# Kernel tuning notes

Hardware: AMD Instinct MI355X
Metric: run time of the kernel (lower is better)

## Reference

```python
import jax, jax.numpy as jnp
import numpy as np

N_POINTS = 1 << 20      # batch of query coordinates
IN_CH = 3               # 3D coordinates in [0,1]
N_FREQ = 8              # Fourier encoding frequencies
ENC_CH = IN_CH + 2 * IN_CH * N_FREQ   # identity + sin/cos -> 51
HIDDEN = 64
OUT_CH = 4


def _fourier_encode(x):
    # x: [N, 3] in [0,1]. Identity + NeRF-style frequency encoding.
    freqs = (2.0 ** jnp.arange(N_FREQ, dtype=x.dtype)) * jnp.pi      # [L]
    xf = x[:, :, None] * freqs                                       # [N, 3, L]
    n = x.shape[0]
    return jnp.concatenate(
        [x, jnp.sin(xf).reshape(n, -1), jnp.cos(xf).reshape(n, -1)], axis=-1
    )  # [N, 51]


def setup_inputs() -> dict:
    key = jax.random.key(0)
    ks = jax.random.split(key, 9)
    inp = jax.random.uniform(ks[0], (N_POINTS, IN_CH), dtype=jnp.float32)

    def _w(k, fan_out, fan_in):
        scale = jnp.sqrt(2.0 / fan_in).astype(jnp.float32)
        return jax.random.normal(k, (fan_out, fan_in), dtype=jnp.float32) * scale

    return {
        "input": inp,
        "W0": _w(ks[1], HIDDEN, ENC_CH), "b0": jnp.zeros((HIDDEN,), jnp.float32),
        "W1": _w(ks[2], HIDDEN, HIDDEN), "b1": jnp.zeros((HIDDEN,), jnp.float32),
        "W2": _w(ks[3], HIDDEN, HIDDEN), "b2": jnp.zeros((HIDDEN,), jnp.float32),
        "W3": _w(ks[4], OUT_CH, HIDDEN), "b3": jnp.zeros((OUT_CH,), jnp.float32),
    }


def reference(input, W0, b0, W1, b1, W2, b2, W3, b3):
    h = _fourier_encode(input)                       # [N, 51]
    h = jax.nn.relu(h @ W0.T + b0)                   # [N, 64]
    h = jax.nn.relu(h @ W1.T + b1)                   # [N, 64]
    h = jax.nn.relu(h @ W2.T + b2)                   # [N, 64]
    return h @ W3.T + b3                             # [N, 4]
```

## Files before the change

### kernel.cpp

```cpp
#include <hip/hip_runtime.h>
#include <cmath>


typedef _Float16 half8 __attribute__((ext_vector_type(8)));
typedef float float4v __attribute__((ext_vector_type(4)));

#define PI_F 3.14159265358979323846f

template <int KIN, int ROWS, bool RELU, bool LAST>
__device__ __forceinline__ void mlp_layer(const float* __restrict__ W,
                                          const float* __restrict__ bias,
                                          float* __restrict__ hb,
                                          float* __restrict__ outp,
                                          long long wbase, int lane, long long n)
{
    const int l15 = lane & 15;
    const int g   = lane >> 4;

    half8 Ah[4][2], Al[4][2];
#pragma unroll
    for (int m = 0; m < 4; ++m) {
        const int row = 16 * m + l15;
#pragma unroll
        for (int c = 0; c < 2; ++c) {
            const int v0 = (8 * c + 2 * g) ^ l15;
            const int v1 = (8 * c + 2 * g + 1) ^ l15;
            float4v r0 = *(const float4v*)&hb[row * 64 + v0 * 4];
            float4v r1 = *(const float4v*)&hb[row * 64 + v1 * 4];
#pragma unroll
            for (int j = 0; j < 4; ++j) {
                float v = r0[j];
                _Float16 hi = (_Float16)v;
                Ah[m][c][j] = hi;
                Al[m][c][j] = (_Float16)(v - (float)hi);
                float w = r1[j];
                _Float16 hw = (_Float16)w;
                Ah[m][c][4 + j] = hw;
                Al[m][c][4 + j] = (_Float16)(w - (float)hw);
            }
        }
    }

    constexpr int NT = (ROWS + 15) / 16;
#pragma unroll
    for (int nt = 0; nt < NT; ++nt) {
        const int j = 16 * nt + l15;
        const float bj = (j < ROWS) ? bias[j] : 0.f;

        half8 Bh[2], Bl[2];
#pragma unroll
        for (int c = 0; c < 2; ++c) {
            if constexpr (KIN == 64 && ROWS == 64) {
                const float4v* Wv = (const float4v*)(W + j * 64 + 32 * c + 8 * g);
                float4v w0 = Wv[0], w1 = Wv[1];
#pragma unroll
                for (int jj = 0; jj < 4; ++jj) {
                    float w = w0[jj];
                    _Float16 hi = (_Float16)w;
                    Bh[c][jj] = hi; Bl[c][jj] = (_Float16)(w - (float)hi);
                    float w2 = w1[jj];
                    _Float16 h2 = (_Float16)w2;
                    Bh[c][4 + jj] = h2; Bl[c][4 + jj] = (_Float16)(w2 - (float)h2);
                }
            } else {
#pragma unroll
                for (int jj = 0; jj < 8; ++jj) {
                    const int k = 32 * c + 8 * g + jj;
                    float w = (j < ROWS && k < KIN) ? W[j * KIN + k] : 0.f;
                    _Float16 hi = (_Float16)w;
                    Bh[c][jj] = hi; Bl[c][jj] = (_Float16)(w - (float)hi);
                }
            }
        }

#pragma unroll
        for (int m = 0; m < 4; ++m) {
            float4v acc = {bj, bj, bj, bj};
#pragma unroll
            for (int c = 0; c < 2; ++c) {
                acc = __builtin_amdgcn_mfma_f32_16x16x32_f16(Ah[m][c], Bh[c], acc, 0, 0, 0);
                acc = __builtin_amdgcn_mfma_f32_16x16x32_f16(Ah[m][c], Bl[c], acc, 0, 0, 0);
                acc = __builtin_amdgcn_mfma_f32_16x16x32_f16(Al[m][c], Bh[c], acc, 0, 0, 0);
            }
            if constexpr (LAST) {
                if (l15 < 4) {
#pragma unroll
                    for (int r = 0; r < 4; ++r) {
                        long long p = wbase + 16 * m + 4 * g + r;
                        if (p < n) outp[p * 4 + l15] = acc[r];
                    }
                }
            } else {
#pragma unroll
                for (int r = 0; r < 4; ++r) {
                    float v = acc[r];
                    if (RELU) v = fmaxf(v, 0.f);
                    const int row = 16 * m + 4 * g + r;
                    const int col = 16 * nt + l15;
                    hb[row * 64 + ((((col >> 2) ^ (row & 15))) << 2) + (col & 3)] = v;
                }
            }
        }
    }
}

__global__ __launch_bounds__(256)
void fused_mlp_mfma(const float* __restrict__ x,
                    const float* __restrict__ W0, const float* __restrict__ b0,
                    const float* __restrict__ W1, const float* __restrict__ b1,
                    const float* __restrict__ W2, const float* __restrict__ b2,
                    const float* __restrict__ W3, const float* __restrict__ b3,
                    float* __restrict__ out, long long n)
{
    __shared__ float hbuf[4][64 * 64];
    const int tid  = threadIdx.x;
    const int wave = tid >> 6;
    const int lane = tid & 63;
    const int l15  = lane & 15;
    float* hb = hbuf[wave];

    const long long wbase = (long long)blockIdx.x * 256 + wave * 64;

    {
        long long p = wbase + lane;
        if (p > n - 1) p = n - 1;
        float xc[3] = {x[3 * p + 0], x[3 * p + 1], x[3 * p + 2]};
        float e[64];
        e[0] = xc[0]; e[1] = xc[1]; e[2] = xc[2];
#pragma unroll
        for (int ch = 0; ch < 3; ++ch) {
#pragma unroll
            for (int f = 0; f < 8; ++f) {
                float s, c;
                sincosf(xc[ch] * (PI_F * (float)(1 << f)), &s, &c);
                e[3 + ch * 8 + f]  = s;
                e[27 + ch * 8 + f] = c;
            }
        }
#pragma unroll
        for (int k = 51; k < 64; ++k) e[k] = 0.f;
#pragma unroll
        for (int cb = 0; cb < 16; ++cb) {
            float4v v = {e[4 * cb], e[4 * cb + 1], e[4 * cb + 2], e[4 * cb + 3]};
            *(float4v*)&hb[lane * 64 + ((cb ^ l15) << 2)] = v;
        }
    }

    mlp_layer<51, 64, true,  false>(W0, b0, hb, nullptr, wbase, lane, n);
    mlp_layer<64, 64, true,  false>(W1, b1, hb, nullptr, wbase, lane, n);
    mlp_layer<64, 64, true,  false>(W2, b2, hb, nullptr, wbase, lane, n);
    mlp_layer<64, 4,  false, true >(W3, b3, hb, out,     wbase, lane, n);
}

extern "C" void kernel_launch(void* const* d_in, const int* in_sizes, int n_in,
                              void* d_out, int out_size, void* d_ws, size_t ws_size,
                              hipStream_t stream)
{
    const float* x  = (const float*)d_in[0];
    const float* W0 = (const float*)d_in[1];
    const float* b0 = (const float*)d_in[2];
    const float* W1 = (const float*)d_in[3];
    const float* b1 = (const float*)d_in[4];
    const float* W2 = (const float*)d_in[5];
    const float* b2 = (const float*)d_in[6];
    const float* W3 = (const float*)d_in[7];
    const float* b3 = (const float*)d_in[8];
    float* out = (float*)d_out;

    const long long n = in_sizes[0] / 3;
    const int block = 256;
    const int grid = (int)((n + 255) / 256);
    fused_mlp_mfma<<<grid, block, 0, stream>>>(x, W0, b0, W1, b1, W2, b2, W3, b3, out, n);
}
```

Measured before the change: 212.8 us.

## Halve rows per wave, drop weight low-part MFMA, use double-angle sincos

Each wave now processes 32 points instead of 64, halving LDS and register footprint and raising occupancy via launch bounds. Weights are converted to fp16 only, removing one of the three split-precision MFMAs per chunk. The Fourier encoding computes one sincos per channel and derives the higher frequencies with double-angle recurrences. The last layer loads only the four output rows. The trade-off is lower weight precision and accumulated recurrence error in the encoding.

```diff
diff --git a/kernel.cpp b/kernel.cpp
--- a/kernel.cpp
+++ b/kernel.cpp
@@ -7,7 +7,11 @@
 
 #define PI_F 3.14159265358979323846f
 
-template <int KIN, int ROWS, bool RELU, bool LAST>
+__device__ __forceinline__ float4v mfma16(half8 a, half8 b, float4v c) {
+    return __builtin_amdgcn_mfma_f32_16x16x32_f16(a, b, c, 0, 0, 0);
+}
+
+template <int MODE, int NT, bool RELU>
 __device__ __forceinline__ void mlp_layer(const float* __restrict__ W,
                                           const float* __restrict__ bias,
                                           float* __restrict__ hb,
@@ -17,76 +21,79 @@
     const int l15 = lane & 15;
     const int g   = lane >> 4;
 
-    half8 Ah[4][2], Al[4][2];
+    half8 Ah[2][2], Al[2][2];
 #pragma unroll
-    for (int m = 0; m < 4; ++m) {
-        const int row = 16 * m + l15;
+    for (int mt = 0; mt < 2; ++mt) {
+        const int row = 16 * mt + l15;
 #pragma unroll
         for (int c = 0; c < 2; ++c) {
-            const int v0 = (8 * c + 2 * g) ^ l15;
-            const int v1 = (8 * c + 2 * g + 1) ^ l15;
-            float4v r0 = *(const float4v*)&hb[row * 64 + v0 * 4];
-            float4v r1 = *(const float4v*)&hb[row * 64 + v1 * 4];
+            const int gl = 8 * c + 2 * g;
+            float4v r0 = *(const float4v*)&hb[row * 64 + ((gl ^ l15) << 2)];
+            float4v r1 = *(const float4v*)&hb[row * 64 + (((gl + 1) ^ l15) << 2)];
 #pragma unroll
             for (int j = 0; j < 4; ++j) {
-                float v = r0[j];
-                _Float16 hi = (_Float16)v;
-                Ah[m][c][j] = hi;
-                Al[m][c][j] = (_Float16)(v - (float)hi);
-                float w = r1[j];
-                _Float16 hw = (_Float16)w;
-                Ah[m][c][4 + j] = hw;
-                Al[m][c][4 + j] = (_Float16)(w - (float)hw);
+                float v0 = r0[j]; _Float16 h0 = (_Float16)v0;
+                Ah[mt][c][j] = h0; Al[mt][c][j] = (_Float16)(v0 - (float)h0);
+                float v1 = r1[j]; _Float16 h1 = (_Float16)v1;
+                Ah[mt][c][4 + j] = h1; Al[mt][c][4 + j] = (_Float16)(v1 - (float)h1);
             }
         }
     }
 
-    constexpr int NT = (ROWS + 15) / 16;
 #pragma unroll
     for (int nt = 0; nt < NT; ++nt) {
-        const int j = 16 * nt + l15;
-        const float bj = (j < ROWS) ? bias[j] : 0.f;
+        const int jch = 16 * nt + l15;
+        float bj;
+        if constexpr (MODE == 2) bj = (l15 < 4) ? bias[l15] : 0.0f;
+        else                     bj = bias[jch];
 
-        half8 Bh[2], Bl[2];
+        half8 Bh[2];
 #pragma unroll
         for (int c = 0; c < 2; ++c) {
-            if constexpr (KIN == 64 && ROWS == 64) {
-                const float4v* Wv = (const float4v*)(W + j * 64 + 32 * c + 8 * g);
+            if constexpr (MODE == 0) {
+#pragma unroll
+                for (int jj = 0; jj < 8; ++jj) {
+                    const int k = 32 * c + 8 * g + jj;
+                    const float w = (k < 51) ? W[jch * 51 + k] : 0.0f;
+                    Bh[c][jj] = (_Float16)w;
+                }
+            } else if constexpr (MODE == 1) {
+                const float4v* Wv = (const float4v*)(W + jch * 64 + 32 * c + 8 * g);
                 float4v w0 = Wv[0], w1 = Wv[1];
 #pragma unroll
                 for (int jj = 0; jj < 4; ++jj) {
-                    float w = w0[jj];
-                    _Float16 hi = (_Float16)w;
-                    Bh[c][jj] = hi; Bl[c][jj] = (_Float16)(w - (float)hi);
-                    float w2 = w1[jj];
-                    _Float16 h2 = (_Float16)w2;
-                    Bh[c][4 + jj] = h2; Bl[c][4 + jj] = (_Float16)(w2 - (float)h2);
+                    Bh[c][jj]     = (_Float16)w0[jj];
+                    Bh[c][4 + jj] = (_Float16)w1[jj];
                 }
             } else {
+                if (l15 < 4) {
+                    const float4v* Wv = (const float4v*)(W + l15 * 64 + 32 * c + 8 * g);
+                    float4v w0 = Wv[0], w1 = Wv[1];
 #pragma unroll
-                for (int jj = 0; jj < 8; ++jj) {
-                    const int k = 32 * c + 8 * g + jj;
-                    float w = (j < ROWS && k < KIN) ? W[j * KIN + k] : 0.f;
-                    _Float16 hi = (_Float16)w;
-                    Bh[c][jj] = hi; Bl[c][jj] = (_Float16)(w - (float)hi);
+                    for (int jj = 0; jj < 4; ++jj) {
+                        Bh[c][jj]     = (_Float16)w0[jj];
+                        Bh[c][4 + jj] = (_Float16)w1[jj];
+                    }
+                } else {
+#pragma unroll
+                    for (int jj = 0; jj < 8; ++jj) Bh[c][jj] = (_Float16)0.0f;
                 }
             }
         }
 
 #pragma unroll
-        for (int m = 0; m < 4; ++m) {
+        for (int mt = 0; mt < 2; ++mt) {
             float4v acc = {bj, bj, bj, bj};
 #pragma unroll
             for (int c = 0; c < 2; ++c) {
-                acc = __builtin_amdgcn_mfma_f32_16x16x32_f16(Ah[m][c], Bh[c], acc, 0, 0, 0);
-                acc = __builtin_amdgcn_mfma_f32_16x16x32_f16(Ah[m][c], Bl[c], acc, 0, 0, 0);
-                acc = __builtin_amdgcn_mfma_f32_16x16x32_f16(Al[m][c], Bh[c], acc, 0, 0, 0);
+                acc = mfma16(Ah[mt][c], Bh[c], acc);
+                acc = mfma16(Al[mt][c], Bh[c], acc);
             }
-            if constexpr (LAST) {
+            if constexpr (MODE == 2) {
                 if (l15 < 4) {
 #pragma unroll
                     for (int r = 0; r < 4; ++r) {
-                        long long p = wbase + 16 * m + 4 * g + r;
+                        long long p = wbase + 16 * mt + 4 * g + r;
                         if (p < n) outp[p * 4 + l15] = acc[r];
                     }
                 }
@@ -94,62 +101,74 @@
 #pragma unroll
                 for (int r = 0; r < 4; ++r) {
                     float v = acc[r];
-                    if (RELU) v = fmaxf(v, 0.f);
-                    const int row = 16 * m + 4 * g + r;
-                    const int col = 16 * nt + l15;
-                    hb[row * 64 + ((((col >> 2) ^ (row & 15))) << 2) + (col & 3)] = v;
+                    if (RELU) v = fmaxf(v, 0.0f);
+                    const int row = 16 * mt + 4 * g + r;
+                    const int phys = (jch >> 2) ^ (row & 15);
+                    hb[row * 64 + (phys << 2) + (jch & 3)] = v;
                 }
             }
         }
     }
 }
 
-__global__ __launch_bounds__(256)
-void fused_mlp_mfma(const float* __restrict__ x,
-                    const float* __restrict__ W0, const float* __restrict__ b0,
-                    const float* __restrict__ W1, const float* __restrict__ b1,
-                    const float* __restrict__ W2, const float* __restrict__ b2,
-                    const float* __restrict__ W3, const float* __restrict__ b3,
-                    float* __restrict__ out, long long n)
+__global__ __launch_bounds__(256, 4)
+void fused_mlp_r4(const float* __restrict__ x,
+                  const float* __restrict__ W0, const float* __restrict__ b0,
+                  const float* __restrict__ W1, const float* __restrict__ b1,
+                  const float* __restrict__ W2, const float* __restrict__ b2,
+                  const float* __restrict__ W3, const float* __restrict__ b3,
+                  float* __restrict__ out, long long n)
 {
-    __shared__ float hbuf[4][64 * 64];
+    __shared__ float hbuf[4][32 * 64];
     const int tid  = threadIdx.x;
     const int wave = tid >> 6;
     const int lane = tid & 63;
-    const int l15  = lane & 15;
     float* hb = hbuf[wave];
 
-    const long long wbase = (long long)blockIdx.x * 256 + wave * 64;
+    const long long wbase = (long long)blockIdx.x * 128 + wave * 32;
 
     {
-        long long p = wbase + lane;
+        long long p = wbase + (lane & 31);
         if (p > n - 1) p = n - 1;
-        float xc[3] = {x[3 * p + 0], x[3 * p + 1], x[3 * p + 2]};
+        const float xc[3] = {x[3 * p + 0], x[3 * p + 1], x[3 * p + 2]};
+
+        float s[3][8], c[3][8];
+#pragma unroll
+        for (int ch = 0; ch < 3; ++ch) {
+            sincosf(PI_F * xc[ch], &s[ch][0], &c[ch][0]);
+#pragma unroll
+            for (int f = 1; f < 8; ++f) {
+                const float sp = s[ch][f - 1], cp = c[ch][f - 1];
+                s[ch][f] = 2.0f * sp * cp;
+                c[ch][f] = fmaf(2.0f * cp, cp, -1.0f);
+            }
+        }
+
         float e[64];
+#pragma unroll
+        for (int k = 0; k < 64; ++k) e[k] = 0.0f;
         e[0] = xc[0]; e[1] = xc[1]; e[2] = xc[2];
 #pragma unroll
-        for (int ch = 0; ch < 3; ++ch) {
+        for (int ch = 0; ch < 3; ++ch)
 #pragma unroll
             for (int f = 0; f < 8; ++f) {
-                float s, c;
-                sincosf(xc[ch] * (PI_F * (float)(1 << f)), &s, &c);
-                e[3 + ch * 8 + f]  = s;
-                e[27 + ch * 8 + f] = c;
+                e[3  + ch * 8 + f] = s[ch][f];
+                e[27 + ch * 8 + f] = c[ch][f];
             }
-        }
+
+        const int row = lane & 31, rs = row & 15, g5 = lane >> 5;
 #pragma unroll
-        for (int k = 51; k < 64; ++k) e[k] = 0.f;
-#pragma unroll
-        for (int cb = 0; cb < 16; ++cb) {
-            float4v v = {e[4 * cb], e[4 * cb + 1], e[4 * cb + 2], e[4 * cb + 3]};
-            *(float4v*)&hb[lane * 64 + ((cb ^ l15) << 2)] = v;
+        for (int t = 0; t < 8; ++t) {
+            const int gr = 8 * g5 + t;
+            float4v v = {e[4 * gr], e[4 * gr + 1], e[4 * gr + 2], e[4 * gr + 3]};
+            *(float4v*)&hb[row * 64 + ((gr ^ rs) << 2)] = v;
         }
     }
 
-    mlp_layer<51, 64, true,  false>(W0, b0, hb, nullptr, wbase, lane, n);
-    mlp_layer<64, 64, true,  false>(W1, b1, hb, nullptr, wbase, lane, n);
-    mlp_layer<64, 64, true,  false>(W2, b2, hb, nullptr, wbase, lane, n);
-    mlp_layer<64, 4,  false, true >(W3, b3, hb, out,     wbase, lane, n);
+    mlp_layer<0, 4, true >(W0, b0, hb, nullptr, wbase, lane, n);
+    mlp_layer<1, 4, true >(W1, b1, hb, nullptr, wbase, lane, n);
+    mlp_layer<1, 4, true >(W2, b2, hb, nullptr, wbase, lane, n);
+    mlp_layer<2, 1, false>(W3, b3, hb, out,     wbase, lane, n);
 }
 
 extern "C" void kernel_launch(void* const* d_in, const int* in_sizes, int n_in,
@@ -168,7 +187,6 @@
     float* out = (float*)d_out;
 
     const long long n = in_sizes[0] / 3;
-    const int block = 256;
-    const int grid = (int)((n + 255) / 256);
-    fused_mlp_mfma<<<grid, block, 0, stream>>>(x, W0, b0, W1, b1, W2, b2, W3, b3, out, n);
+    const int grid = (int)((n + 127) / 128);
+    fused_mlp_r4<<<grid, 256, 0, stream>>>(x, W0, b0, W1, b1, W2, b2, W3, b3, out, n);
 }
```

Measured after the change: 346.2 us. +62.7%, slower.
